# Kernel tuning notes

Measured on AMD Instinct MI355X. Metric: run time of the kernel, lower is better.

## Reference

```python
import jax, jax.numpy as jnp
import numpy as np
from jax import lax

M = 512      # num_centers
K = 32       # neighbors per center
FEAT = 256   # token feature dim
EPS = 1e-5   # BatchNorm eps


def fps(xyz, m):
    """Furthest point sampling. xyz: (B,N,3) -> idx (B,m) int32."""
    B, N, _ = xyz.shape
    first = jnp.zeros((B,), jnp.int32)

    def step(carry, _):
        min_d, last = carry                       # (B,N), (B,)
        last_pt = jnp.take_along_axis(xyz, last[:, None, None], axis=1)  # (B,1,3)
        d = jnp.sum((xyz - last_pt) ** 2, axis=-1)                       # (B,N)
        min_d = jnp.minimum(min_d, d)
        nxt = jnp.argmax(min_d, axis=1).astype(jnp.int32)
        return (min_d, nxt), nxt

    init = (jnp.full((B, N), 1e10, jnp.float32), first)
    _, rest = lax.scan(step, init, None, length=m - 1)   # (m-1, B)
    return jnp.concatenate([first[None, :], rest], axis=0).T  # (B,m)


def bn(x, g, b, mean, var):
    return (x - mean) * (g * lax.rsqrt(var + EPS)) + b


def setup_inputs() -> dict:
    key = jax.random.key(0)
    ks = jax.random.split(key, 16)
    B, N = 8, 16384
    r = lambda k_, s, sc=0.1: jax.random.normal(k_, s, jnp.float32) * sc
    inp = {
        "xyz": jax.random.normal(ks[0], (B, N, 3), jnp.float32),
        "W1": r(ks[1], (64, 3)), "b1": r(ks[2], (64,)),
        "g1": 1.0 + r(ks[3], (64,)), "be1": r(ks[4], (64,)),
        "m1": r(ks[5], (64,)), "v1": 1.0 + 0.1 * jax.random.uniform(ks[6], (64,)),
        "W2": r(ks[7], (128, 64)), "b2": r(ks[8], (128,)),
        "g2": 1.0 + r(ks[9], (128,)), "be2": r(ks[10], (128,)),
        "m2": r(ks[11], (128,)), "v2": 1.0 + 0.1 * jax.random.uniform(ks[12], (128,)),
        "W3": r(ks[13], (FEAT, 128)), "b3": r(ks[14], (FEAT,)),
        "Wp": r(ks[15], (FEAT, 3)), "bp": jnp.zeros((FEAT,), jnp.float32),
    }
    return inp


def reference(xyz, W1, b1, g1, be1, m1, v1, W2, b2, g2, be2, m2, v2, W3, b3, Wp, bp):
    B, N, _ = xyz.shape
    # --- FPS centers ---
    idx_c = fps(xyz, M)                                            # (B,M)
    centers = jnp.take_along_axis(xyz, idx_c[:, :, None], axis=1)  # (B,M,3)
    # --- brute-force KNN ---
    dist = jnp.sum((centers[:, :, None, :] - xyz[:, None, :, :]) ** 2, axis=-1)  # (B,M,N)
    _, idx = lax.top_k(-dist, K)                                   # (B,M,K)
    nbrs = jnp.take_along_axis(
        xyz, idx.reshape(B, M * K)[:, :, None], axis=1
    ).reshape(B, M, K, 3)
    grouped = nbrs - centers[:, :, None, :]                        # (B,M,K,3)
    # --- MiniPointNet: 1x1 convs == channel matmuls, eval-mode BN ---
    h = jnp.einsum("bmkc,oc->bmko", grouped, W1) + b1
    h = jax.nn.relu(bn(h, g1, be1, m1, v1))
    h = jnp.einsum("bmkc,oc->bmko", h, W2) + b2
    h = jax.nn.relu(bn(h, g2, be2, m2, v2))
    h = jnp.einsum("bmkc,oc->bmko", h, W3) + b3
    tokens = jnp.max(h, axis=2)                                    # (B,M,FEAT)
    pos = jnp.einsum("bmc,oc->bmo", centers, Wp) + bp
    return centers, tokens + pos
```

## Files before the change

kernel.cpp:

```cpp
#include <hip/hip_runtime.h>

typedef unsigned int u32;
typedef unsigned long long u64;
typedef unsigned short u16;

#define DEVFN static __device__ __forceinline__

constexpr int NPTS = 16384;
constexpr int NC = 512;

typedef __attribute__((ext_vector_type(8))) short bf16x8;
typedef __attribute__((ext_vector_type(4))) float f32x4;

#define MFMA16(a, b, c) __builtin_amdgcn_mfma_f32_16x16x32_bf16(a, b, c, 0, 0, 0)

DEVFN u16 bf16rne(float f) {
  u32 b = __float_as_uint(f);
  u32 r = (b + 0x7FFFu + ((b >> 16) & 1u)) >> 16;
  return (u16)r;
}

DEVFN u64 shflx64(u64 v, int m) {
  u32 lo = __shfl_xor((u32)v, m, 64);
  u32 hi = __shfl_xor((u32)(v >> 32), m, 64);
  return ((u64)hi << 32) | lo;
}
DEVFN u64 shfl64(u64 v, int src) {
  u32 lo = __shfl((u32)v, src, 64);
  u32 hi = __shfl((u32)(v >> 32), src, 64);
  return ((u64)hi << 32) | lo;
}

DEVFN void csw(u64& a, u64& b) {
  u64 lo = a < b ? a : b;
  u64 hi = a < b ? b : a;
  a = lo; b = hi;
}

DEVFN u32 spread3(u32 v) {
  return (v & 1u) | ((v & 2u) << 2) | ((v & 4u) << 4) | ((v & 8u) << 6);
}

template <int CTRL, int RM>
DEVFN u64 dppmax64(u64 k) {
  u32 lo = (u32)k, hi = (u32)(k >> 32);
  u32 lo2 = (u32)__builtin_amdgcn_update_dpp((int)lo, (int)lo, CTRL, RM, 0xF, false);
  u32 hi2 = (u32)__builtin_amdgcn_update_dpp((int)hi, (int)hi, CTRL, RM, 0xF, false);
  u64 o = ((u64)hi2 << 32) | lo2;
  return o > k ? o : k;
}
DEVFN u64 wavemax64(u64 k) {
  k = dppmax64<0x121, 0xF>(k);
  k = dppmax64<0x122, 0xF>(k);
  k = dppmax64<0x124, 0xF>(k);
  k = dppmax64<0x128, 0xF>(k);
  k = dppmax64<0x142, 0xA>(k);
  k = dppmax64<0x143, 0xC>(k);
  return k;
}

__global__ __launch_bounds__(1024) void fps_kernel(const float* __restrict__ xyz,
                                                   float* __restrict__ centers,
                                                   float* __restrict__ wsX,
                                                   float* __restrict__ wsY,
                                                   float* __restrict__ wsZ,
                                                   u16* __restrict__ wsO) {
  const int b = blockIdx.x;
  const int t = threadIdx.x;
  const int lane = t & 63;
  const int w = t >> 6;
  const float* xb = xyz + (size_t)b * NPTS * 3;
  const int bo = b * NPTS;

  __shared__ char smem[75776];
  float* mdL = (float*)smem;
  u64* ckeyL = (u64*)(smem + 65536);
  float* bboxT = (float*)(smem + 67584);
  u16* wl = (u16*)(smem + 73728);
  u32* wcnt = (u32*)(smem + 74752);
  float* redB = (float*)(smem + 74768);
  u32* redW = (u32*)(smem + 75200);
  u32* hist = (u32*)smem;
  u16* soidx = (u16*)(smem + 8192);

  const u32 inf10 = __float_as_uint(1e10f);

  u32 mcode[16];
  {
    float ox[16], oy[16], oz[16];
    float lx = 1e30f, ly = 1e30f, lz = 1e30f;
    float hx = -1e30f, hy = -1e30f, hz = -1e30f;
#pragma unroll
    for (int j = 0; j < 16; ++j) {
      int p = t + j * 1024;
      ox[j] = xb[p * 3 + 0];
      oy[j] = xb[p * 3 + 1];
      oz[j] = xb[p * 3 + 2];
      lx = fminf(lx, ox[j]); hx = fmaxf(hx, ox[j]);
      ly = fminf(ly, oy[j]); hy = fmaxf(hy, oy[j]);
      lz = fminf(lz, oz[j]); hz = fmaxf(hz, oz[j]);
    }
#pragma unroll
    for (int s = 32; s; s >>= 1) {
      lx = fminf(lx, __shfl_xor(lx, s, 64)); hx = fmaxf(hx, __shfl_xor(hx, s, 64));
      ly = fminf(ly, __shfl_xor(ly, s, 64)); hy = fmaxf(hy, __shfl_xor(hy, s, 64));
      lz = fminf(lz, __shfl_xor(lz, s, 64)); hz = fmaxf(hz, __shfl_xor(hz, s, 64));
    }
    if (lane == 0) {
      redB[w * 6 + 0] = lx; redB[w * 6 + 1] = hx;
      redB[w * 6 + 2] = ly; redB[w * 6 + 3] = hy;
      redB[w * 6 + 4] = lz; redB[w * 6 + 5] = hz;
    }
    hist[t] = 0; hist[t + 1024] = 0;
    if (t < 2) wcnt[t] = 0;
    __syncthreads();
    if (t == 0) {
      float a0 = redB[0], a1 = redB[1], a2 = redB[2], a3 = redB[3], a4 = redB[4], a5 = redB[5];
      for (int q = 1; q < 16; ++q) {
        a0 = fminf(a0, redB[q * 6 + 0]); a1 = fmaxf(a1, redB[q * 6 + 1]);
        a2 = fminf(a2, redB[q * 6 + 2]); a3 = fmaxf(a3, redB[q * 6 + 3]);
        a4 = fminf(a4, redB[q * 6 + 4]); a5 = fmaxf(a5, redB[q * 6 + 5]);
      }
      redB[96] = a0; redB[97] = a1; redB[98] = a2;
      redB[99] = a3; redB[100] = a4; redB[101] = a5;
    }
    __syncthreads();
    const float glx = redB[96], ghx = redB[97];
    const float gly = redB[98], ghy = redB[99];
    const float glz = redB[100], ghz = redB[101];
    const float sx = 15.999f / fmaxf(ghx - glx, 1e-9f);
    const float sy = 15.999f / fmaxf(ghy - gly, 1e-9f);
    const float sz = 7.999f / fmaxf(ghz - glz, 1e-9f);
#pragma unroll
    for (int j = 0; j < 16; ++j) {
      int ix = min(15, max(0, (int)((ox[j] - glx) * sx)));
      int iy = min(15, max(0, (int)((oy[j] - gly) * sy)));
      int iz = min(7, max(0, (int)((oz[j] - glz) * sz)));
      mcode[j] = spread3((u32)ix) | (spread3((u32)iy) << 1) | (spread3((u32)iz) << 2);
    }
  }
#pragma unroll
  for (int j = 0; j < 16; ++j) atomicAdd(&hist[mcode[j]], 1u);
  __syncthreads();
  {
    u32 h0 = hist[t * 2 + 0], h1 = hist[t * 2 + 1];
    u32 s = h0 + h1;
    u32 incl = s;
#pragma unroll
    for (int d = 1; d < 64; d <<= 1) {
      u32 n = __shfl_up(incl, d, 64);
      if (lane >= d) incl += n;
    }
    if (lane == 63) redW[w] = incl;
    __syncthreads();
    if (t == 0) {
      u32 run = 0;
      for (int q = 0; q < 16; ++q) { u32 tmp = redW[q]; redW[q] = run; run += tmp; }
    }
    __syncthreads();
    u32 exc = incl - s + redW[w];
    hist[t * 2 + 0] = exc;
    hist[t * 2 + 1] = exc + h0;
    __syncthreads();
  }
#pragma unroll
  for (int j = 0; j < 16; ++j) {
    u32 p = (u32)(t + j * 1024);
    u32 pos = atomicAdd(&hist[mcode[j]], 1u);
    soidx[pos] = (u16)p;
  }
  __syncthreads();
  {
    const int c = t >> 2;
    const int q = t & 3;
    float bxl = 1e30f, bxh = -1e30f, byl = 1e30f, byh = -1e30f, bzl = 1e30f, bzh = -1e30f;
    u32 lomax = 0;
#pragma unroll
    for (int j = 0; j < 16; ++j) {
      int sp = c * 64 + q * 16 + j;
      u32 oidx = (u32)soidx[sp];
      float X = xb[oidx * 3 + 0];
      float Y = xb[oidx * 3 + 1];
      float Z = xb[oidx * 3 + 2];
      wsX[bo + sp] = X; wsY[bo + sp] = Y; wsZ[bo + sp] = Z;
      wsO[bo + sp] = (u16)oidx;
      lomax = max(lomax, 16383u - oidx);
      bxl = fminf(bxl, X); bxh = fmaxf(bxh, X);
      byl = fminf(byl, Y); byh = fmaxf(byh, Y);
      bzl = fminf(bzl, Z); bzh = fmaxf(bzh, Z);
    }
#pragma unroll
    for (int s = 1; s <= 2; s <<= 1) {
      bxl = fminf(bxl, __shfl_xor(bxl, s, 64)); bxh = fmaxf(bxh, __shfl_xor(bxh, s, 64));
      byl = fminf(byl, __shfl_xor(byl, s, 64)); byh = fmaxf(byh, __shfl_xor(byh, s, 64));
      bzl = fminf(bzl, __shfl_xor(bzl, s, 64)); bzh = fmaxf(bzh, __shfl_xor(bzh, s, 64));
      lomax = max(lomax, (u32)__shfl_xor(lomax, s, 64));
    }
    if (q == 0) {
      bboxT[0 * 256 + c] = bxl; bboxT[1 * 256 + c] = bxh;
      bboxT[2 * 256 + c] = byl; bboxT[3 * 256 + c] = byh;
      bboxT[4 * 256 + c] = bzl; bboxT[5 * 256 + c] = bzh;
      ckeyL[c] = ((u64)inf10 << 32) | lomax;
    }
  }
  __syncthreads();
#pragma unroll
  for (int j = 0; j < 16; ++j) mdL[t + j * 1024] = 1e10f;

  float cx = xb[0], cy = xb[1], cz = xb[2];
  if (t == 0) {
    centers[(b * NC) * 3 + 0] = cx;
    centers[(b * NC) * 3 + 1] = cy;
    centers[(b * NC) * 3 + 2] = cz;
  }

  for (int i = 1; i < NC; ++i) {
    if (t < 256) {
      float mdm = __uint_as_float((u32)(ckeyL[t] >> 32));
      float ax = fmaxf(0.f, fmaxf(__fsub_rn(bboxT[0 * 256 + t], cx), __fsub_rn(cx, bboxT[1 * 256 + t])));
      float ay = fmaxf(0.f, fmaxf(__fsub_rn(bboxT[2 * 256 + t], cy), __fsub_rn(cy, bboxT[3 * 256 + t])));
      float az = fmaxf(0.f, fmaxf(__fsub_rn(bboxT[4 * 256 + t], cz), __fsub_rn(cz, bboxT[5 * 256 + t])));
      float dlb = __fadd_rn(__fadd_rn(__fmul_rn(ax, ax), __fmul_rn(ay, ay)), __fmul_rn(az, az));
      if (dlb < mdm) {
        u32 pos = atomicAdd(&wcnt[i & 1], 1u);
        wl[(i & 1) * 256 + pos] = (u16)t;
      }
    } else if (t == 512) {
      wcnt[(i + 1) & 1] = 0u;
    }
    __syncthreads();
    {
      const int A = (int)wcnt[i & 1];
      for (int e = w; e < A; e += 16) {
        const int c = (int)wl[(i & 1) * 256 + e];
        const int sp = c * 64 + lane;
        float X = wsX[bo + sp];
        float Y = wsY[bo + sp];
        float Z = wsZ[bo + sp];
        u32 oidx = (u32)wsO[bo + sp];
        float dx = __fsub_rn(X, cx);
        float dy = __fsub_rn(Y, cy);
        float dz = __fsub_rn(Z, cz);
        float d = __fadd_rn(__fadd_rn(__fmul_rn(dx, dx), __fmul_rn(dy, dy)), __fmul_rn(dz, dz));
        float nm = fminf(mdL[sp], d);
        mdL[sp] = nm;
        u64 key = ((u64)__float_as_uint(nm) << 32) | (16383u - oidx);
        key = wavemax64(key);
        if (lane == 63) ckeyL[c] = key;
      }
    }
    __syncthreads();
    {
      u64 g0 = ckeyL[lane];
      u64 g1 = ckeyL[lane + 64];
      u64 g2 = ckeyL[lane + 128];
      u64 g3 = ckeyL[lane + 192];
      u64 g = g0 > g1 ? g0 : g1;
      u64 h = g2 > g3 ? g2 : g3;
      g = g > h ? g : h;
      g = wavemax64(g);
      u32 glo = (u32)__builtin_amdgcn_readlane((int)(u32)g, 63);
      u32 oidx = 16383u - glo;
      cx = xb[oidx * 3 + 0];
      cy = xb[oidx * 3 + 1];
      cz = xb[oidx * 3 + 2];
      if (t == 0) {
        centers[(b * NC + i) * 3 + 0] = cx;
        centers[(b * NC + i) * 3 + 1] = cy;
        centers[(b * NC + i) * 3 + 2] = cz;
      }
    }
  }
}

__global__ __launch_bounds__(512) void knn_kernel(const float* __restrict__ xyz,
                                                  const float* __restrict__ centers,
                                                  float* __restrict__ grouped) {
  __shared__ float spts[1024 * 3];
  __shared__ u64 cand[8][192];
  __shared__ int ccnt[8];
  const int t = threadIdx.x;
  const int lane = t & 63;
  const int w = t >> 6;
  const int cg = blockIdx.x * 8 + w;
  const int b = cg >> 9;
  const float* xb = xyz + (size_t)b * NPTS * 3;
  const float cx = centers[cg * 3 + 0];
  const float cy = centers[cg * 3 + 1];
  const float cz = centers[cg * 3 + 2];
  if (lane == 0) ccnt[w] = 0;

  u64 lmin = ~0ull;
  for (int ch = 0; ch < 16; ++ch) {
    __syncthreads();
    const float* src = xb + ch * 1024 * 3;
#pragma unroll
    for (int q = 0; q < 6; ++q) spts[q * 512 + t] = src[q * 512 + t];
    __syncthreads();
#pragma unroll
    for (int j = 0; j < 16; ++j) {
      int p = lane + j * 64;
      float dx = __fsub_rn(cx, spts[p * 3 + 0]);
      float dy = __fsub_rn(cy, spts[p * 3 + 1]);
      float dz = __fsub_rn(cz, spts[p * 3 + 2]);
      float d = __fadd_rn(__fadd_rn(__fmul_rn(dx, dx), __fmul_rn(dy, dy)), __fmul_rn(dz, dz));
      u64 kk = ((u64)__float_as_uint(d) << 32) | (u64)(u32)(ch * 1024 + p);
      lmin = kk < lmin ? kk : lmin;
    }
  }
  u64 v = lmin;
  for (int k = 2; k <= 64; k <<= 1)
    for (int j = k >> 1; j > 0; j >>= 1) {
      u64 o = shflx64(v, j);
      bool up = ((lane & k) == 0);
      bool lowr = ((lane & j) == 0);
      u64 mn = v < o ? v : o;
      u64 mx = v < o ? o : v;
      v = (lowr == up) ? mn : mx;
    }
  u64 tau = shfl64(v, 31);
  float tf = __uint_as_float((u32)(tau >> 32));

  for (int ch = 0; ch < 16; ++ch) {
    __syncthreads();
    const float* src = xb + ch * 1024 * 3;
#pragma unroll
    for (int q = 0; q < 6; ++q) spts[q * 512 + t] = src[q * 512 + t];
    __syncthreads();
#pragma unroll
    for (int j = 0; j < 16; ++j) {
      int p = lane + j * 64;
      float dx = __fsub_rn(cx, spts[p * 3 + 0]);
      float dy = __fsub_rn(cy, spts[p * 3 + 1]);
      float dz = __fsub_rn(cz, spts[p * 3 + 2]);
      float d = __fadd_rn(__fadd_rn(__fmul_rn(dx, dx), __fmul_rn(dy, dy)), __fmul_rn(dz, dz));
      if (d <= tf) {
        int pos = atomicAdd(&ccnt[w], 1);
        if (pos < 192) cand[w][pos] = ((u64)__float_as_uint(d) << 32) | (u64)(u32)(ch * 1024 + p);
      }
    }
  }
  __syncthreads();
  int cnt = ccnt[w];
  u32 myn = 0u;
  if (cnt <= 192) {
    u64 c0 = (lane < cnt) ? cand[w][lane] : ~0ull;
    u64 c1 = (64 + lane < cnt) ? cand[w][64 + lane] : ~0ull;
    u64 c2 = (128 + lane < cnt) ? cand[w][128 + lane] : ~0ull;
    csw(c0, c1); csw(c1, c2); csw(c0, c1);
    for (int r = 0; r < 32; ++r) {
      u64 wm = c0;
      for (int s = 32; s; s >>= 1) {
        u64 o = shflx64(wm, s);
        wm = o < wm ? o : wm;
      }
      if (c0 == wm) { c0 = c1; c1 = c2; c2 = ~0ull; }
      if (lane == r) myn = (u32)wm;
    }
  } else {
    u64 last = 0ull;
    for (int r = 0; r < 32; ++r) {
      u64 bb = ~0ull;
      for (int j = 0; j < 256; ++j) {
        int p = lane + j * 64;
        float dx = __fsub_rn(cx, xb[p * 3 + 0]);
        float dy = __fsub_rn(cy, xb[p * 3 + 1]);
        float dz = __fsub_rn(cz, xb[p * 3 + 2]);
        float d = __fadd_rn(__fadd_rn(__fmul_rn(dx, dx), __fmul_rn(dy, dy)), __fmul_rn(dz, dz));
        u64 kk = ((u64)__float_as_uint(d) << 32) | (u64)(u32)p;
        if (r == 0 || kk > last)
          if (kk < bb) bb = kk;
      }
      for (int s = 32; s; s >>= 1) {
        u64 o = shflx64(bb, s);
        bb = o < bb ? o : bb;
      }
      last = bb;
      if (lane == r) myn = (u32)bb;
    }
  }
  if (lane < 32) {
    const float nx = xb[(size_t)myn * 3 + 0];
    const float ny = xb[(size_t)myn * 3 + 1];
    const float nz = xb[(size_t)myn * 3 + 2];
    float* gp = grouped + ((size_t)cg * 32 + lane) * 3;
    gp[0] = __fsub_rn(nx, cx);
    gp[1] = __fsub_rn(ny, cy);
    gp[2] = __fsub_rn(nz, cz);
  }
}

__global__ __launch_bounds__(256) void prep_kernel(
    const float* __restrict__ W1, const float* __restrict__ b1,
    const float* __restrict__ g1, const float* __restrict__ be1,
    const float* __restrict__ m1, const float* __restrict__ v1,
    const float* __restrict__ W2, const float* __restrict__ b2,
    const float* __restrict__ g2, const float* __restrict__ be2,
    const float* __restrict__ m2, const float* __restrict__ v2,
    const float* __restrict__ W3,
    float* __restrict__ w1eff, u16* __restrict__ w2L,
    float* __restrict__ t2, u16* __restrict__ w3L) {
  const int tid = blockIdx.x * 256 + threadIdx.x;
  if (tid < 64) {
    float s = g1[tid] / sqrtf(v1[tid] + 1e-5f);
    w1eff[tid * 4 + 0] = W1[tid * 3 + 0] * s;
    w1eff[tid * 4 + 1] = W1[tid * 3 + 1] * s;
    w1eff[tid * 4 + 2] = W1[tid * 3 + 2] * s;
    w1eff[tid * 4 + 3] = (b1[tid] - m1[tid]) * s + be1[tid];
  }
  if (tid < 128) {
    float s = g2[tid] / sqrtf(v2[tid] + 1e-5f);
    t2[tid] = (b2[tid] - m2[tid]) * s + be2[tid];
  }
  if (tid < 8192) {
    int i = tid & 63, o = tid >> 6;
    float s = g2[o] / sqrtf(v2[o] + 1e-5f);
    int kg = i >> 3, j = i & 7;
    w2L[((((kg * 128) + o) * 8) ^ ((kg & 7) * 8)) + j] = bf16rne(W2[o * 64 + i] * s);
  }
  if (tid < 32768) {
    int i = tid & 127, o = tid >> 7;
    int kg = i >> 3, j = i & 7;
    int h = o >> 7, colh = o & 127;
    w3L[h * 16384 + ((((kg * 128) + colh) * 8) ^ ((kg & 7) * 8)) + j] = bf16rne(W3[o * 128 + i]);
  }
}

__global__ __launch_bounds__(256) void mlp_kernel(
    const float* __restrict__ grouped, const u16* __restrict__ w2L,
    const u16* __restrict__ w3L, const float* __restrict__ w1eff,
    const float* __restrict__ t2, const float* __restrict__ b3,
    const float* __restrict__ Wp, const float* __restrict__ bp,
    const float* __restrict__ centers, float* __restrict__ tokens) {
  __shared__ char lds[65536];
  const int t = threadIdx.x;
  const int lane = t & 63;
  const int w = t >> 6;
  const int l15 = lane & 15;
  const int lg = lane >> 4;
  const int c0 = blockIdx.x * 4;
  {
    const u32* s = (const u32*)w2L;
    u32* d = (u32*)lds;
#pragma unroll
    for (int q = 0; q < 16; ++q) d[q * 256 + t] = s[q * 256 + t];
  }
  {
    const int row = t & 127;
    const int oh = (t >> 7) * 32;
    const int cg = c0 + (row >> 5);
    const float* gp = grouped + ((size_t)cg * 32 + (row & 31)) * 3;
    const float gx = gp[0], gy = gp[1], gz = gp[2];
    u16 hv[32];
#pragma unroll
    for (int o = 0; o < 32; ++o) {
      const float4 wvv = ((const float4*)w1eff)[oh + o];
      float h = fmaxf(0.f, gx * wvv.x + gy * wvv.y + gz * wvv.z + wvv.w);
      hv[o] = bf16rne(h);
    }
#pragma unroll
    for (int c4 = 0; c4 < 4; ++c4) {
      uint4 pk;
      pk.x = (u32)hv[c4 * 8 + 0] | ((u32)hv[c4 * 8 + 1] << 16);
      pk.y = (u32)hv[c4 * 8 + 2] | ((u32)hv[c4 * 8 + 3] << 16);
      pk.z = (u32)hv[c4 * 8 + 4] | ((u32)hv[c4 * 8 + 5] << 16);
      pk.w = (u32)hv[c4 * 8 + 6] | ((u32)hv[c4 * 8 + 7] << 16);
      int byte = row * 128 + oh * 2 + c4 * 16;
      *reinterpret_cast<uint4*>(lds + 16384 + (byte ^ ((row & 7) << 4))) = pk;
    }
  }
  __syncthreads();
  f32x4 acc2[2][8];
#pragma unroll
  for (int m = 0; m < 2; ++m)
#pragma unroll
    for (int n = 0; n < 8; ++n) acc2[m][n] = (f32x4){0.f, 0.f, 0.f, 0.f};
#pragma unroll
  for (int ks = 0; ks < 2; ++ks) {
    bf16x8 a[2];
#pragma unroll
    for (int m = 0; m < 2; ++m) {
      int row = w * 32 + m * 16 + l15;
      int byte = row * 128 + (ks * 32 + lg * 8) * 2;
      a[m] = *reinterpret_cast<const bf16x8*>(lds + 16384 + (byte ^ ((row & 7) << 4)));
    }
    const int kg = ks * 4 + lg;
#pragma unroll
    for (int n = 0; n < 8; ++n) {
      int idx = (((kg * 128) + (n * 16 + l15)) * 8) ^ ((kg & 7) * 8);
      bf16x8 bb = *reinterpret_cast<const bf16x8*>((const u16*)lds + idx);
      acc2[0][n] = MFMA16(a[0], bb, acc2[0][n]);
      acc2[1][n] = MFMA16(a[1], bb, acc2[1][n]);
    }
  }
#pragma unroll
  for (int n = 0; n < 8; ++n) {
    const int col = n * 16 + l15;
    const float t2v = t2[col];
#pragma unroll
    for (int m = 0; m < 2; ++m)
#pragma unroll
      for (int r = 0; r < 4; ++r) {
        float vv = fmaxf(0.f, acc2[m][n][r] + t2v);
        int row = w * 32 + m * 16 + lg * 4 + r;
        int byte = row * 256 + col * 2;
        *reinterpret_cast<u16*>(lds + 32768 + (byte ^ ((row & 7) << 4))) = bf16rne(vv);
      }
  }
  __syncthreads();
  const float ccx = centers[(c0 + w) * 3 + 0];
  const float ccy = centers[(c0 + w) * 3 + 1];
  const float ccz = centers[(c0 + w) * 3 + 2];
  float* tok = tokens + (size_t)(c0 + w) * 256;
  for (int h = 0; h < 2; ++h) {
    {
      const u32* s = (const u32*)w3L + h * 8192;
      u32* d = (u32*)lds;
#pragma unroll
      for (int q = 0; q < 32; ++q) d[q * 256 + t] = s[q * 256 + t];
    }
    __syncthreads();
    f32x4 acc3[2][8];
#pragma unroll
    for (int m = 0; m < 2; ++m)
#pragma unroll
      for (int n = 0; n < 8; ++n) acc3[m][n] = (f32x4){0.f, 0.f, 0.f, 0.f};
#pragma unroll
    for (int ks = 0; ks < 4; ++ks) {
      bf16x8 a[2];
#pragma unroll
      for (int m = 0; m < 2; ++m) {
        int row = w * 32 + m * 16 + l15;
        int byte = row * 256 + (ks * 32 + lg * 8) * 2;
        a[m] = *reinterpret_cast<const bf16x8*>(lds + 32768 + (byte ^ ((row & 7) << 4)));
      }
      const int kg = ks * 4 + lg;
#pragma unroll
      for (int n = 0; n < 8; ++n) {
        int idx = (((kg * 128) + (n * 16 + l15)) * 8) ^ ((kg & 7) * 8);
        bf16x8 bb = *reinterpret_cast<const bf16x8*>((const u16*)lds + idx);
        acc3[0][n] = MFMA16(a[0], bb, acc3[0][n]);
        acc3[1][n] = MFMA16(a[1], bb, acc3[1][n]);
      }
    }
#pragma unroll
    for (int n = 0; n < 8; ++n) {
      float vmx = acc3[0][n][0];
#pragma unroll
      for (int m = 0; m < 2; ++m)
#pragma unroll
        for (int r = 0; r < 4; ++r) vmx = fmaxf(vmx, acc3[m][n][r]);
      vmx = fmaxf(vmx, __shfl_xor(vmx, 16, 64));
      vmx = fmaxf(vmx, __shfl_xor(vmx, 32, 64));
      const int col = h * 128 + n * 16 + l15;
      if (lane < 16) {
        float pos = Wp[col * 3 + 0] * ccx + Wp[col * 3 + 1] * ccy +
                    Wp[col * 3 + 2] * ccz + bp[col] + b3[col];
        tok[col] = vmx + pos;
      }
    }
    __syncthreads();
  }
}

extern "C" void kernel_launch(void* const* d_in, const int* in_sizes, int n_in,
                              void* d_out, int out_size, void* d_ws, size_t ws_size,
                              hipStream_t stream) {
  const float* xyz = (const float*)d_in[0];
  const float* W1 = (const float*)d_in[1];
  const float* b1 = (const float*)d_in[2];
  const float* g1 = (const float*)d_in[3];
  const float* be1 = (const float*)d_in[4];
  const float* m1 = (const float*)d_in[5];
  const float* v1 = (const float*)d_in[6];
  const float* W2 = (const float*)d_in[7];
  const float* b2 = (const float*)d_in[8];
  const float* g2 = (const float*)d_in[9];
  const float* be2 = (const float*)d_in[10];
  const float* m2 = (const float*)d_in[11];
  const float* v2 = (const float*)d_in[12];
  const float* W3 = (const float*)d_in[13];
  const float* b3 = (const float*)d_in[14];
  const float* Wp = (const float*)d_in[15];
  const float* bp = (const float*)d_in[16];

  char* ws = (char*)d_ws;
  float* wsX = (float*)ws;
  float* wsY = (float*)(ws + 524288);
  float* wsZ = (float*)(ws + 1048576);
  u16* wsO = (u16*)(ws + 1572864);
  float* grouped = (float*)ws;
  float* w1eff = (float*)(ws + 1835008);
  u16* w2L = (u16*)(ws + 1836032);
  float* t2 = (float*)(ws + 1852416);
  u16* w3L = (u16*)(ws + 1852928);

  float* centers = (float*)d_out;
  float* tokens = (float*)d_out + 8 * 512 * 3;

  prep_kernel<<<dim3(128), dim3(256), 0, stream>>>(W1, b1, g1, be1, m1, v1,
                                                   W2, b2, g2, be2, m2, v2, W3,
                                                   w1eff, w2L, t2, w3L);
  fps_kernel<<<dim3(8), dim3(1024), 0, stream>>>(xyz, centers, wsX, wsY, wsZ, wsO);
  knn_kernel<<<dim3(512), dim3(512), 0, stream>>>(xyz, centers, grouped);
  mlp_kernel<<<dim3(1024), dim3(256), 0, stream>>>(grouped, w2L, w3L, w1eff, t2,
                                                   b3, Wp, bp, centers, tokens);
}
```

Before: 844.7 us.

## Pack FPS point data as float4 and cache cell winner coordinates in LDS

Stores sorted points as one float4 per point (xyz plus a packed key holding the inverted index and the cell id) instead of separate X/Y/Z/index arrays, so each active cell does one vector load. Each cell's winning point coordinates are kept in shared memory, so the serial step that picks the next center reads LDS instead of doing a dependent global gather. The 64-bit max reductions use fmax on doubles, which relies on the positive float distance in the high word giving the same ordering. This adds readlanes and compare-and-store work per wave, grows LDS use, and moves the workspace offsets for the other buffers.

Measured after the change: 832.6 us. No clear change (-1.4%).

```diff
diff --git a/kernel.cpp b/kernel.cpp
--- a/kernel.cpp
+++ b/kernel.cpp
@@ -41,30 +41,31 @@
   return (v & 1u) | ((v & 2u) << 2) | ((v & 4u) << 4) | ((v & 8u) << 6);
 }
 
+DEVFN u64 maxf64u(u64 a, u64 b) {
+  double x = __longlong_as_double((long long)a);
+  double y = __longlong_as_double((long long)b);
+  return (u64)__double_as_longlong(fmax(x, y));
+}
 template <int CTRL, int RM>
-DEVFN u64 dppmax64(u64 k) {
+DEVFN u64 dppmaxf(u64 k) {
   u32 lo = (u32)k, hi = (u32)(k >> 32);
   u32 lo2 = (u32)__builtin_amdgcn_update_dpp((int)lo, (int)lo, CTRL, RM, 0xF, false);
   u32 hi2 = (u32)__builtin_amdgcn_update_dpp((int)hi, (int)hi, CTRL, RM, 0xF, false);
-  u64 o = ((u64)hi2 << 32) | lo2;
-  return o > k ? o : k;
-}
-DEVFN u64 wavemax64(u64 k) {
-  k = dppmax64<0x121, 0xF>(k);
-  k = dppmax64<0x122, 0xF>(k);
-  k = dppmax64<0x124, 0xF>(k);
-  k = dppmax64<0x128, 0xF>(k);
-  k = dppmax64<0x142, 0xA>(k);
-  k = dppmax64<0x143, 0xC>(k);
+  return maxf64u(k, ((u64)hi2 << 32) | lo2);
+}
+DEVFN u64 wavemaxf(u64 k) {
+  k = dppmaxf<0x121, 0xF>(k);
+  k = dppmaxf<0x122, 0xF>(k);
+  k = dppmaxf<0x124, 0xF>(k);
+  k = dppmaxf<0x128, 0xF>(k);
+  k = dppmaxf<0x142, 0xA>(k);
+  k = dppmaxf<0x143, 0xC>(k);
   return k;
 }
 
 __global__ __launch_bounds__(1024) void fps_kernel(const float* __restrict__ xyz,
                                                    float* __restrict__ centers,
-                                                   float* __restrict__ wsX,
-                                                   float* __restrict__ wsY,
-                                                   float* __restrict__ wsZ,
-                                                   u16* __restrict__ wsO) {
+                                                   float4* __restrict__ ws4) {
   const int b = blockIdx.x;
   const int t = threadIdx.x;
   const int lane = t & 63;
@@ -72,14 +73,15 @@
   const float* xb = xyz + (size_t)b * NPTS * 3;
   const int bo = b * NPTS;
 
-  __shared__ char smem[75776];
+  __shared__ char smem[78336];
   float* mdL = (float*)smem;
   u64* ckeyL = (u64*)(smem + 65536);
   float* bboxT = (float*)(smem + 67584);
-  u16* wl = (u16*)(smem + 73728);
-  u32* wcnt = (u32*)(smem + 74752);
-  float* redB = (float*)(smem + 74768);
-  u32* redW = (u32*)(smem + 75200);
+  float* ccoordL = (float*)(smem + 73728);
+  u16* wl = (u16*)(smem + 76800);
+  u32* wcnt = (u32*)(smem + 77824);
+  float* redB = (float*)(smem + 77832);
+  u32* redW = (u32*)(smem + 78248);
   u32* hist = (u32*)smem;
   u16* soidx = (u16*)(smem + 8192);
 
@@ -175,6 +177,7 @@
     const int q = t & 3;
     float bxl = 1e30f, bxh = -1e30f, byl = 1e30f, byh = -1e30f, bzl = 1e30f, bzh = -1e30f;
     u32 lomax = 0;
+    float axc = 0.f, ayc = 0.f, azc = 0.f;
 #pragma unroll
     for (int j = 0; j < 16; ++j) {
       int sp = c * 64 + q * 16 + j;
@@ -182,25 +185,30 @@
       float X = xb[oidx * 3 + 0];
       float Y = xb[oidx * 3 + 1];
       float Z = xb[oidx * 3 + 2];
-      wsX[bo + sp] = X; wsY[bo + sp] = Y; wsZ[bo + sp] = Z;
-      wsO[bo + sp] = (u16)oidx;
-      lomax = max(lomax, 16383u - oidx);
+      u32 lo = ((16383u - oidx) << 8) | (u32)c;
+      float4 pk; pk.x = X; pk.y = Y; pk.z = Z; pk.w = __uint_as_float(lo);
+      ws4[bo + sp] = pk;
+      if (lo > lomax) { lomax = lo; axc = X; ayc = Y; azc = Z; }
       bxl = fminf(bxl, X); bxh = fmaxf(bxh, X);
       byl = fminf(byl, Y); byh = fmaxf(byh, Y);
       bzl = fminf(bzl, Z); bzh = fmaxf(bzh, Z);
     }
+    u32 gl = lomax;
 #pragma unroll
     for (int s = 1; s <= 2; s <<= 1) {
       bxl = fminf(bxl, __shfl_xor(bxl, s, 64)); bxh = fmaxf(bxh, __shfl_xor(bxh, s, 64));
       byl = fminf(byl, __shfl_xor(byl, s, 64)); byh = fmaxf(byh, __shfl_xor(byh, s, 64));
       bzl = fminf(bzl, __shfl_xor(bzl, s, 64)); bzh = fmaxf(bzh, __shfl_xor(bzh, s, 64));
-      lomax = max(lomax, (u32)__shfl_xor(lomax, s, 64));
+      gl = max(gl, (u32)__shfl_xor(gl, s, 64));
+    }
+    if (lomax == gl) {
+      ccoordL[c * 3 + 0] = axc; ccoordL[c * 3 + 1] = ayc; ccoordL[c * 3 + 2] = azc;
     }
     if (q == 0) {
       bboxT[0 * 256 + c] = bxl; bboxT[1 * 256 + c] = bxh;
       bboxT[2 * 256 + c] = byl; bboxT[3 * 256 + c] = byh;
       bboxT[4 * 256 + c] = bzl; bboxT[5 * 256 + c] = bzh;
-      ckeyL[c] = ((u64)inf10 << 32) | lomax;
+      ckeyL[c] = ((u64)inf10 << 32) | gl;
     }
   }
   __syncthreads();
@@ -234,19 +242,22 @@
       for (int e = w; e < A; e += 16) {
         const int c = (int)wl[(i & 1) * 256 + e];
         const int sp = c * 64 + lane;
-        float X = wsX[bo + sp];
-        float Y = wsY[bo + sp];
-        float Z = wsZ[bo + sp];
-        u32 oidx = (u32)wsO[bo + sp];
-        float dx = __fsub_rn(X, cx);
-        float dy = __fsub_rn(Y, cy);
-        float dz = __fsub_rn(Z, cz);
+        float4 p = ws4[bo + sp];
+        float dx = __fsub_rn(p.x, cx);
+        float dy = __fsub_rn(p.y, cy);
+        float dz = __fsub_rn(p.z, cz);
         float d = __fadd_rn(__fadd_rn(__fmul_rn(dx, dx), __fmul_rn(dy, dy)), __fmul_rn(dz, dz));
         float nm = fminf(mdL[sp], d);
         mdL[sp] = nm;
-        u64 key = ((u64)__float_as_uint(nm) << 32) | (16383u - oidx);
-        key = wavemax64(key);
-        if (lane == 63) ckeyL[c] = key;
+        u64 key = ((u64)__float_as_uint(nm) << 32) | (u64)__float_as_uint(p.w);
+        u64 r = wavemaxf(key);
+        u32 klo = (u32)__builtin_amdgcn_readlane((int)(u32)r, 63);
+        u32 khi = (u32)__builtin_amdgcn_readlane((int)(u32)(r >> 32), 63);
+        u64 wmax = ((u64)khi << 32) | klo;
+        if (key == wmax) {
+          ckeyL[c] = key;
+          ccoordL[c * 3 + 0] = p.x; ccoordL[c * 3 + 1] = p.y; ccoordL[c * 3 + 2] = p.z;
+        }
       }
     }
     __syncthreads();
@@ -255,15 +266,13 @@
       u64 g1 = ckeyL[lane + 64];
       u64 g2 = ckeyL[lane + 128];
       u64 g3 = ckeyL[lane + 192];
-      u64 g = g0 > g1 ? g0 : g1;
-      u64 h = g2 > g3 ? g2 : g3;
-      g = g > h ? g : h;
-      g = wavemax64(g);
+      u64 g = maxf64u(maxf64u(g0, g1), maxf64u(g2, g3));
+      g = wavemaxf(g);
       u32 glo = (u32)__builtin_amdgcn_readlane((int)(u32)g, 63);
-      u32 oidx = 16383u - glo;
-      cx = xb[oidx * 3 + 0];
-      cy = xb[oidx * 3 + 1];
-      cz = xb[oidx * 3 + 2];
+      u32 widx = glo & 255u;
+      cx = ccoordL[widx * 3 + 0];
+      cy = ccoordL[widx * 3 + 1];
+      cz = ccoordL[widx * 3 + 2];
       if (t == 0) {
         centers[(b * NC + i) * 3 + 0] = cx;
         centers[(b * NC + i) * 3 + 1] = cy;
@@ -585,15 +594,12 @@
   const float* bp = (const float*)d_in[16];
 
   char* ws = (char*)d_ws;
-  float* wsX = (float*)ws;
-  float* wsY = (float*)(ws + 524288);
-  float* wsZ = (float*)(ws + 1048576);
-  u16* wsO = (u16*)(ws + 1572864);
+  float4* ws4 = (float4*)ws;
   float* grouped = (float*)ws;
-  float* w1eff = (float*)(ws + 1835008);
-  u16* w2L = (u16*)(ws + 1836032);
-  float* t2 = (float*)(ws + 1852416);
-  u16* w3L = (u16*)(ws + 1852928);
+  float* w1eff = (float*)(ws + 2097152);
+  u16* w2L = (u16*)(ws + 2098176);
+  float* t2 = (float*)(ws + 2114560);
+  u16* w3L = (u16*)(ws + 2115072);
 
   float* centers = (float*)d_out;
   float* tokens = (float*)d_out + 8 * 512 * 3;
@@ -601,7 +607,7 @@
   prep_kernel<<<dim3(128), dim3(256), 0, stream>>>(W1, b1, g1, be1, m1, v1,
                                                    W2, b2, g2, be2, m2, v2, W3,
                                                    w1eff, w2L, t2, w3L);
-  fps_kernel<<<dim3(8), dim3(1024), 0, stream>>>(xyz, centers, wsX, wsY, wsZ, wsO);
+  fps_kernel<<<dim3(8), dim3(1024), 0, stream>>>(xyz, centers, ws4);
   knn_kernel<<<dim3(512), dim3(512), 0, stream>>>(xyz, centers, grouped);
   mlp_kernel<<<dim3(1024), dim3(256), 0, stream>>>(grouped, w2L, w3L, w1eff, t2,
                                                    b3, Wp, bp, centers, tokens);
```
